# Performance work log

Measured on AMD Instinct MI355X. Metric: run time of the kernel, lower is better.

The kernel has to match this reference:

```python
import jax, jax.numpy as jnp
import numpy as np

C = 512
H = 8
D = C // H
GROUPS = 32
EPS = 1e-5

def setup_inputs() -> dict:
    key = jax.random.key(0)
    ks = jax.random.split(key, 7)
    B, L = 4, 2048
    x = jax.random.normal(ks[0], (B, C, L), dtype=jnp.float32)
    gamma = jnp.ones((C,), dtype=jnp.float32)
    beta = jnp.zeros((C,), dtype=jnp.float32)
    w_qkv = jax.random.normal(ks[1], (3 * C, C), dtype=jnp.float32) * (1.0 / np.sqrt(C))
    b_qkv = jax.random.normal(ks[2], (3 * C,), dtype=jnp.float32) * 0.01
    w_proj = jax.random.normal(ks[3], (C, C), dtype=jnp.float32) * (1.0 / np.sqrt(C))
    b_proj = jax.random.normal(ks[4], (C,), dtype=jnp.float32) * 0.01
    return {"x": x, "gamma": gamma, "beta": beta, "w_qkv": w_qkv,
            "b_qkv": b_qkv, "w_proj": w_proj, "b_proj": b_proj}

def _group_norm(x, gamma, beta):
    B, Cc, L = x.shape
    xg = x.reshape(B, GROUPS, Cc // GROUPS, L)
    mean = jnp.mean(xg, axis=(2, 3), keepdims=True)
    var = jnp.var(xg, axis=(2, 3), keepdims=True)
    xn = ((xg - mean) * jax.lax.rsqrt(var + EPS)).reshape(B, Cc, L)
    return xn * gamma[None, :, None] + beta[None, :, None]

def reference(x, gamma, beta, w_qkv, b_qkv, w_proj, b_proj):
    B, Cc, L = x.shape
    h = _group_norm(x, gamma, beta)
    # 1x1 conv == channel matmul: (3C,C) x (B,C,L) -> (B,3C,L)
    qkv = jnp.einsum('oc,bcl->bol', w_qkv, h) + b_qkv[None, :, None]
    q, k, v = jnp.split(qkv, 3, axis=1)
    # (B,C,L) -> (B,H,L,D)
    def to_heads(t):
        return t.reshape(B, H, D, L).transpose(0, 1, 3, 2)
    q, k, v = to_heads(q), to_heads(k), to_heads(v)
    scale = 1.0 / np.sqrt(D).astype(np.float32)
    attn = jnp.einsum('bhqd,bhkd->bhqk', q, k) * scale  # [B,H,L,L]
    attn = jax.nn.softmax(attn, axis=-1)
    out = jnp.einsum('bhqk,bhkd->bhqd', attn, v)  # [B,H,L,D]
    out = out.transpose(0, 1, 3, 2).reshape(B, Cc, L)
    proj = jnp.einsum('oc,bcl->bol', w_proj, out) + b_proj[None, :, None]
    return x + proj
```

## Files before the change

kernel.cpp:

```cpp
#include <hip/hip_runtime.h>
#include <stdint.h>

#define C_DIM 512
#define H_HEADS 8
#define D_HEAD 64
#define B_BATCH 4
#define L_SEQ 2048
#define GROUPS 32
#define EPS_GN 1e-5f

typedef unsigned short u16;
typedef __attribute__((ext_vector_type(8))) __bf16 bf16x8;
typedef __attribute__((ext_vector_type(2))) float f32x2;
typedef __attribute__((ext_vector_type(4))) float f32x4;
typedef __attribute__((ext_vector_type(16))) float f32x16;

__device__ __forceinline__ u16 f2bf(float f) {
  unsigned u = __builtin_bit_cast(unsigned, f);
  unsigned r = u + 0x7FFFu + ((u >> 16) & 1u);
  return (u16)(r >> 16);
}

__device__ __forceinline__ unsigned cvtpk_bf16(float lo, float hi) {
  unsigned r;
  asm("v_cvt_pk_bf16_f32 %0, %1, %2" : "=v"(r) : "v"(lo), "v"(hi));
  return r;
}

__device__ __forceinline__ void pl32swap(unsigned& a, unsigned& b) {
  asm("v_permlane32_swap_b32 %0, %1" : "+v"(a), "+v"(b));
}

__device__ __forceinline__ bf16x8 mk8(unsigned a, unsigned b, unsigned c, unsigned d) {
  union { uint4 u; bf16x8 v; } z;
  z.u.x = a; z.u.y = b; z.u.z = c; z.u.w = d;
  return z.v;
}

__device__ __forceinline__ void gl16(const void* g, void* l) {
  __builtin_amdgcn_global_load_lds((const __attribute__((address_space(1))) void*)g,
                                   (__attribute__((address_space(3))) void*)l, 16, 0, 0);
}

__global__ __launch_bounds__(256) void prep_kernel(const float* __restrict__ x,
                                                   const float* __restrict__ gamma,
                                                   const float* __restrict__ beta,
                                                   const float* __restrict__ wq,
                                                   const float* __restrict__ wp,
                                                   u16* __restrict__ h_t,
                                                   u16* __restrict__ wq_bf,
                                                   u16* __restrict__ wp_bf) {
  if (blockIdx.x >= 128) {
    int i = (blockIdx.x - 128) * 256 + threadIdx.x;
    const int nq = 3 * C_DIM * C_DIM;
    int idx = i * 4;
    const float* src;
    u16* dst;
    if (idx < nq) { src = wq + idx; dst = wq_bf + idx; }
    else          { src = wp + (idx - nq); dst = wp_bf + (idx - nq); }
    float4 v = *(const float4*)src;
    uint2 pk;
    pk.x = cvtpk_bf16(v.x, v.y);
    pk.y = cvtpk_bf16(v.z, v.w);
    *(uint2*)dst = pk;
    return;
  }
  int bg = blockIdx.x;
  int b = bg >> 5, g = bg & 31;
  const float* base = x + ((size_t)(b * C_DIM + g * 16)) * L_SEQ;
  int t = threadIdx.x;
  int w = t >> 6;
  float s = 0.f, sq = 0.f;
  for (int i = 0; i < 32; ++i) {
    float4 v = ((const float4*)base)[t + i * 256];
    s += v.x + v.y + v.z + v.w;
    sq += v.x * v.x + v.y * v.y + v.z * v.z + v.w * v.w;
  }
  for (int off = 32; off; off >>= 1) { s += __shfl_down(s, off); sq += __shfl_down(sq, off); }
  __shared__ float red[8];
  if ((t & 63) == 0) { red[w * 2] = s; red[w * 2 + 1] = sq; }
  __syncthreads();
  float ts = red[0] + red[2] + red[4] + red[6];
  float tq = red[1] + red[3] + red[5] + red[7];
  float mean = ts * (1.f / 32768.f);
  float var = tq * (1.f / 32768.f) - mean * mean;
  float rstd = rsqrtf(var + EPS_GN);
  float ga[16], be[16];
#pragma unroll
  for (int c = 0; c < 16; ++c) {
    float gm = gamma[g * 16 + c];
    ga[c] = gm * rstd;
    be[c] = beta[g * 16 + c] - mean * gm * rstd;
  }
  __shared__ float tile[16][260];
  for (int lc = 0; lc < 8; ++lc) {
    __syncthreads();
#pragma unroll
    for (int it = 0; it < 4; ++it) {
      int r = it * 4 + w;
      int c4 = (t & 63) * 4;
      *(float4*)&tile[r][c4] = *(const float4*)(base + (size_t)r * L_SEQ + lc * 256 + c4);
    }
    __syncthreads();
    int l = lc * 256 + t;
    unsigned wds[8];
#pragma unroll
    for (int c = 0; c < 8; ++c) {
      float a0 = tile[2 * c][t] * ga[2 * c] + be[2 * c];
      float a1 = tile[2 * c + 1][t] * ga[2 * c + 1] + be[2 * c + 1];
      wds[c] = cvtpk_bf16(a0, a1);
    }
    u16* dst = h_t + ((size_t)(b * L_SEQ + l)) * C_DIM + g * 16;
    uint4 p0; p0.x = wds[0]; p0.y = wds[1]; p0.z = wds[2]; p0.w = wds[3];
    uint4 p1; p1.x = wds[4]; p1.y = wds[5]; p1.z = wds[6]; p1.w = wds[7];
    *(uint4*)dst = p0;
    *(uint4*)(dst + 8) = p1;
  }
}

__global__ __launch_bounds__(256) void gemm_qkv(const u16* __restrict__ A_bf,
                                                const u16* __restrict__ B_t,
                                                const float* __restrict__ bias,
                                                u16* __restrict__ q_t,
                                                u16* __restrict__ kf_g,
                                                u16* __restrict__ vf_g) {
  constexpr int K = 512;
  __shared__ u16 A_lds[128][32];
  __shared__ u16 B_lds[128][32];
  int t = threadIdx.x;
  int w = t >> 6, lane = t & 63;
  int q4 = lane >> 4, c15 = lane & 15;
  int wm = w >> 1, wn = w & 1;
  int o0 = blockIdx.y * 128;
  int l0 = blockIdx.x * 128;
  int b = blockIdx.z;
  const u16* Bb = B_t + (size_t)b * L_SEQ * K;
  f32x4 acc[4][4] = {};

  int sr = lane >> 2, sc = lane & 3;
  int r0 = w * 32 + sr;
  int r1 = r0 + 16;
  int lc0 = (sc - (r0 >> 1)) & 3;
  int lc1 = (sc - (r1 >> 1)) & 3;
  const u16* Ag0 = A_bf + (size_t)(o0 + r0) * K + lc0 * 8;
  const u16* Ag1 = A_bf + (size_t)(o0 + r1) * K + lc1 * 8;
  const u16* Bg0 = Bb + (size_t)(l0 + r0) * K + lc0 * 8;
  const u16* Bg1 = Bb + (size_t)(l0 + r1) * K + lc1 * 8;
  u16* Al0 = &A_lds[w * 32][0];
  u16* Al1 = &A_lds[w * 32 + 16][0];
  u16* Bl0 = &B_lds[w * 32][0];
  u16* Bl1 = &B_lds[w * 32 + 16][0];

  for (int kt = 0; kt < K / 32; ++kt) {
    gl16(Ag0, Al0); gl16(Ag1, Al1);
    gl16(Bg0, Bl0); gl16(Bg1, Bl1);
    Ag0 += 32; Ag1 += 32; Bg0 += 32; Bg1 += 32;
    __syncthreads();
    bf16x8 af[4], bfr[4];
#pragma unroll
    for (int mi = 0; mi < 4; ++mi) {
      int ar = wm * 64 + mi * 16 + c15;
      af[mi] = *(const bf16x8*)&A_lds[ar][((q4 + (ar >> 1)) & 3) * 8];
    }
#pragma unroll
    for (int ni = 0; ni < 4; ++ni) {
      int br = wn * 64 + ni * 16 + c15;
      bfr[ni] = *(const bf16x8*)&B_lds[br][((q4 + (br >> 1)) & 3) * 8];
    }
#pragma unroll
    for (int mi = 0; mi < 4; ++mi)
#pragma unroll
      for (int ni = 0; ni < 4; ++ni)
        acc[mi][ni] = __builtin_amdgcn_mfma_f32_16x16x32_bf16(af[mi], bfr[ni], acc[mi][ni], 0, 0, 0);
    __syncthreads();
  }

  const float QS = 0.18033688f;
  int sel = o0 >> 9;
  int ob = o0 - sel * 512 + wm * 64;
#pragma unroll
  for (int mi = 0; mi < 4; ++mi) {
    int orow = ob + mi * 16 + q4 * 4;
    float4 bi = *(const float4*)&bias[o0 + wm * 64 + mi * 16 + q4 * 4];
#pragma unroll
    for (int ni = 0; ni < 4; ++ni) {
      int l = l0 + wn * 64 + ni * 16 + c15;
      float v0 = acc[mi][ni][0] + bi.x;
      float v1 = acc[mi][ni][1] + bi.y;
      float v2 = acc[mi][ni][2] + bi.z;
      float v3 = acc[mi][ni][3] + bi.w;
      if (sel == 0) {
        v0 *= QS; v1 *= QS; v2 *= QS; v3 *= QS;
        uint2 pk;
        pk.x = cvtpk_bf16(v0, v1);
        pk.y = cvtpk_bf16(v2, v3);
        *(uint2*)(q_t + ((size_t)(b * L_SEQ + l)) * C_DIM + orow) = pk;
      } else if (sel == 1) {
        int hh = orow >> 6, d = orow & 63;
        size_t base = ((size_t)(b * 8 + hh)) * 131072 +
                      (size_t)(((l >> 5) * 4 + (d >> 4))) * 512 +
                      (size_t)((l & 31) + ((d >> 3) & 1) * 32) * 8 + (d & 7);
        uint2 pk;
        pk.x = cvtpk_bf16(v0, v1);
        pk.y = cvtpk_bf16(v2, v3);
        *(uint2*)(kf_g + base) = pk;
      } else {
        int hh = orow >> 6, d = orow & 63;
        size_t base0 = ((size_t)(b * 8 + hh)) * 131072 +
                       (size_t)(l >> 4) * 1024 +
                       (size_t)((l >> 3) & 1) * 256 + (l & 7);
        vf_g[base0 + (size_t)((d + 0) >> 5) * 512 + ((d + 0) & 31) * 8] = f2bf(v0);
        vf_g[base0 + (size_t)((d + 1) >> 5) * 512 + ((d + 1) & 31) * 8] = f2bf(v1);
        vf_g[base0 + (size_t)((d + 2) >> 5) * 512 + ((d + 2) & 31) * 8] = f2bf(v2);
        vf_g[base0 + (size_t)((d + 3) >> 5) * 512 + ((d + 3) & 31) * 8] = f2bf(v3);
      }
    }
  }
}

__global__ __launch_bounds__(256) void gemm_proj(const u16* __restrict__ A_bf,
                                                 const u16* __restrict__ B_t,
                                                 const float* __restrict__ bias,
                                                 const float* __restrict__ xres,
                                                 float* __restrict__ out_f) {
  constexpr int K = 512;
  __shared__ u16 A_lds[64][32];
  __shared__ u16 B_lds[128][32];
  int t = threadIdx.x;
  int w = t >> 6, lane = t & 63;
  int q4 = lane >> 4, c15 = lane & 15;
  int o0 = blockIdx.y * 64;
  int l0 = blockIdx.x * 128;
  int b = blockIdx.z;
  const u16* Bb = B_t + (size_t)b * L_SEQ * K;
  f32x4 acc[4][2] = {};

  int sr = lane >> 2, sc = lane & 3;
  int ra = w * 16 + sr;
  int lca = (sc - (ra >> 1)) & 3;
  const u16* Ag = A_bf + (size_t)(o0 + ra) * K + lca * 8;
  int rb0 = w * 32 + sr, rb1 = rb0 + 16;
  int lcb0 = (sc - (rb0 >> 1)) & 3;
  int lcb1 = (sc - (rb1 >> 1)) & 3;
  const u16* Bg0 = Bb + (size_t)(l0 + rb0) * K + lcb0 * 8;
  const u16* Bg1 = Bb + (size_t)(l0 + rb1) * K + lcb1 * 8;
  u16* Al = &A_lds[w * 16][0];
  u16* Bl0 = &B_lds[w * 32][0];
  u16* Bl1 = &B_lds[w * 32 + 16][0];

  for (int kt = 0; kt < K / 32; ++kt) {
    gl16(Ag, Al);
    gl16(Bg0, Bl0); gl16(Bg1, Bl1);
    Ag += 32; Bg0 += 32; Bg1 += 32;
    __syncthreads();
    bf16x8 af[4], bfr[2];
#pragma unroll
    for (int mi = 0; mi < 4; ++mi) {
      int ar = mi * 16 + c15;
      af[mi] = *(const bf16x8*)&A_lds[ar][((q4 + (ar >> 1)) & 3) * 8];
    }
#pragma unroll
    for (int ni = 0; ni < 2; ++ni) {
      int br = w * 32 + ni * 16 + c15;
      bfr[ni] = *(const bf16x8*)&B_lds[br][((q4 + (br >> 1)) & 3) * 8];
    }
#pragma unroll
    for (int mi = 0; mi < 4; ++mi)
#pragma unroll
      for (int ni = 0; ni < 2; ++ni)
        acc[mi][ni] = __builtin_amdgcn_mfma_f32_16x16x32_bf16(af[mi], bfr[ni], acc[mi][ni], 0, 0, 0);
    __syncthreads();
  }

#pragma unroll
  for (int mi = 0; mi < 4; ++mi) {
    int orow = o0 + mi * 16 + q4 * 4;
    float4 bi = *(const float4*)&bias[orow];
#pragma unroll
    for (int ni = 0; ni < 2; ++ni) {
      int l = l0 + w * 32 + ni * 16 + c15;
      size_t base2 = ((size_t)(b * C_DIM + orow)) * L_SEQ + l;
      out_f[base2] = acc[mi][ni][0] + bi.x + xres[base2];
      out_f[base2 + L_SEQ] = acc[mi][ni][1] + bi.y + xres[base2 + L_SEQ];
      out_f[base2 + 2 * L_SEQ] = acc[mi][ni][2] + bi.z + xres[base2 + 2 * L_SEQ];
      out_f[base2 + 3 * L_SEQ] = acc[mi][ni][3] + bi.w + xres[base2 + 3 * L_SEQ];
    }
  }
}

#define ATILE(KC, KN, T)                                                       \
  {                                                                            \
    int tn = (T) + 1; tn = tn > 31 ? 31 : tn;                                  \
    const u16* kp = kfb + tn * 2048;                                           \
    const u16* vp = vfb + (T) * 2048;                                          \
    KN[0] = *(const bf16x8*)(kp);                                              \
    KN[1] = *(const bf16x8*)(kp + 512);                                        \
    KN[2] = *(const bf16x8*)(kp + 1024);                                       \
    KN[3] = *(const bf16x8*)(kp + 1536);                                       \
    bf16x8 v0 = *(const bf16x8*)(vp);                                          \
    bf16x8 v1 = *(const bf16x8*)(vp + 512);                                    \
    bf16x8 v2 = *(const bf16x8*)(vp + 1024);                                   \
    bf16x8 v3 = *(const bf16x8*)(vp + 1536);                                   \
    f32x16 s;                                                                  \
    _Pragma("unroll") for (int r = 0; r < 16; ++r) s[r] = 0.f;                 \
    s = __builtin_amdgcn_mfma_f32_32x32x16_bf16(KC[0], qf[0], s, 0, 0, 0);     \
    s = __builtin_amdgcn_mfma_f32_32x32x16_bf16(KC[1], qf[1], s, 0, 0, 0);     \
    s = __builtin_amdgcn_mfma_f32_32x32x16_bf16(KC[2], qf[2], s, 0, 0, 0);     \
    s = __builtin_amdgcn_mfma_f32_32x32x16_bf16(KC[3], qf[3], s, 0, 0, 0);     \
    _Pragma("unroll") for (int r = 0; r < 16; ++r)                             \
        s[r] = __builtin_amdgcn_exp2f(s[r]);                                   \
    f32x2 a0_ = {s[0], s[1]}, a1_ = {s[2], s[3]}, a2_ = {s[4], s[5]},          \
          a3_ = {s[6], s[7]}, a4_ = {s[8], s[9]}, a5_ = {s[10], s[11]},        \
          a6_ = {s[12], s[13]}, a7_ = {s[14], s[15]};                          \
    f32x2 b0_ = a0_ + a1_, b1_ = a2_ + a3_, b2_ = a4_ + a5_, b3_ = a6_ + a7_;  \
    f32x2 c0_ = b0_ + b1_, c1_ = b2_ + b3_;                                    \
    f32x2 d0_ = c0_ + c1_;                                                     \
    float sum = d0_[0] + d0_[1];                                               \
    sum += __shfl_xor(sum, 32);                                                \
    l_r += sum;                                                                \
    unsigned pk[8];                                                            \
    _Pragma("unroll") for (int i = 0; i < 8; ++i)                              \
        pk[i] = cvtpk_bf16(s[2 * i], s[2 * i + 1]);                            \
    pl32swap(pk[0], pk[2]); pl32swap(pk[1], pk[3]);                            \
    pl32swap(pk[4], pk[6]); pl32swap(pk[5], pk[7]);                            \
    bf16x8 pf0 = mk8(pk[0], pk[1], pk[2], pk[3]);                              \
    bf16x8 pf1 = mk8(pk[4], pk[5], pk[6], pk[7]);                              \
    o0 = __builtin_amdgcn_mfma_f32_32x32x16_bf16(v0, pf0, o0, 0, 0, 0);        \
    o1 = __builtin_amdgcn_mfma_f32_32x32x16_bf16(v1, pf0, o1, 0, 0, 0);        \
    o0 = __builtin_amdgcn_mfma_f32_32x32x16_bf16(v2, pf1, o0, 0, 0, 0);        \
    o1 = __builtin_amdgcn_mfma_f32_32x32x16_bf16(v3, pf1, o1, 0, 0, 0);        \
  }

__global__ __launch_bounds__(256, 4) void attn_kernel(const u16* __restrict__ q_t,
                                                      const u16* __restrict__ kf_g,
                                                      const u16* __restrict__ vf_g,
                                                      u16* __restrict__ ao_t) {
  __shared__ float oL[4][64][32];
  __shared__ float lL[4][32];

  int g = blockIdx.x;
  int wk = (g & 7) * 128 + (g >> 3);
  int qg = wk & 31, bh = wk >> 5;
  int b = bh >> 3, h = bh & 7;
  int t = threadIdx.x;
  int wv = t >> 6, lane = t & 63;
  int q = lane & 31, hi = lane >> 5;
  int qh = wv & 1, kvh = wv >> 1;
  int q0 = qg * 64 + qh * 32;

  const u16* qp = q_t + ((size_t)(b * L_SEQ + q0 + q)) * C_DIM + h * 64 + hi * 8;
  bf16x8 qf[4];
#pragma unroll
  for (int kk = 0; kk < 4; ++kk) qf[kk] = *(const bf16x8*)(qp + kk * 16);

  const u16* kfb = kf_g + (size_t)bh * 131072 + (size_t)kvh * 65536 + lane * 8;
  const u16* vfb = vf_g + (size_t)bh * 131072 + (size_t)kvh * 65536 + lane * 8;

  f32x16 o0, o1;
#pragma unroll
  for (int r = 0; r < 16; ++r) { o0[r] = 0.f; o1[r] = 0.f; }
  float l_r = 0.f;

  bf16x8 kA[4], kB[4];
#pragma unroll
  for (int i = 0; i < 4; ++i) kA[i] = *(const bf16x8*)(kfb + i * 512);

  for (int it = 0; it < 16; ++it) {
    ATILE(kA, kB, 2 * it);
    ATILE(kB, kA, 2 * it + 1);
  }

  if (hi == 0) lL[wv][q] = l_r;
#pragma unroll
  for (int r = 0; r < 16; ++r) {
    int d = (r & 3) + 8 * (r >> 2) + 4 * hi;
    oL[wv][d][q] = o0[r];
    oL[wv][d + 32][q] = o1[r];
  }
  __syncthreads();

  int tq = t & 31;
  int oqh = (t >> 5) & 1;
  int d0 = (t >> 6) * 16;
  float lsum = lL[oqh][tq] + lL[oqh + 2][tq];
  float inv = 1.f / lsum;
  float v[16];
#pragma unroll
  for (int i = 0; i < 16; ++i)
    v[i] = (oL[oqh][d0 + i][tq] + oL[oqh + 2][d0 + i][tq]) * inv;
  u16* dst = ao_t + ((size_t)(b * L_SEQ + qg * 64 + oqh * 32 + tq)) * C_DIM + h * 64 + d0;
  uint4 ov0, ov1;
  ov0.x = cvtpk_bf16(v[0], v[1]);
  ov0.y = cvtpk_bf16(v[2], v[3]);
  ov0.z = cvtpk_bf16(v[4], v[5]);
  ov0.w = cvtpk_bf16(v[6], v[7]);
  ov1.x = cvtpk_bf16(v[8], v[9]);
  ov1.y = cvtpk_bf16(v[10], v[11]);
  ov1.z = cvtpk_bf16(v[12], v[13]);
  ov1.w = cvtpk_bf16(v[14], v[15]);
  *(uint4*)dst = ov0;
  *(uint4*)(dst + 8) = ov1;
}

extern "C" void kernel_launch(void* const* d_in, const int* in_sizes, int n_in,
                              void* d_out, int out_size, void* d_ws, size_t ws_size,
                              hipStream_t stream) {
  const float* x = (const float*)d_in[0];
  const float* gamma = (const float*)d_in[1];
  const float* beta = (const float*)d_in[2];
  const float* w_qkv = (const float*)d_in[3];
  const float* b_qkv = (const float*)d_in[4];
  const float* w_proj = (const float*)d_in[5];
  const float* b_proj = (const float*)d_in[6];
  float* out = (float*)d_out;

  u16* wq_bf = (u16*)d_ws;
  u16* wp_bf = wq_bf + 786432;
  u16* h_t = wp_bf + 262144;
  u16* q_t = h_t + 4194304;
  u16* kf_g = q_t + 4194304;
  u16* vf_g = kf_g + 4194304;
  u16* ao_t = vf_g + 4194304;

  prep_kernel<<<dim3(1152), dim3(256), 0, stream>>>(x, gamma, beta, w_qkv, w_proj,
                                                    h_t, wq_bf, wp_bf);
  gemm_qkv<<<dim3(16, 12, 4), dim3(256), 0, stream>>>(wq_bf, h_t, b_qkv, q_t, kf_g, vf_g);
  attn_kernel<<<dim3(1024), dim3(256), 0, stream>>>(q_t, kf_g, vf_g, ao_t);
  gemm_proj<<<dim3(16, 8, 4), dim3(256), 0, stream>>>(wp_bf, ao_t, b_proj, x, out);
}
```

Baseline: 103.4 us.

## Software-pipeline QK^T one tile ahead of softmax/PV in attention loop

Restructures the attention inner loop so the QK^T MFMAs for tile T+1 are issued while exp2, row-sum and PV MFMAs for tile T run, and K loads are prefetched two tiles ahead. The goal is to hide MFMA latency and exp/convert dependency chains behind independent matrix work. It keeps an extra 16-float score accumulator live, and launch bounds drop from 4 to 3 waves per SIMD to make room for the registers, which lowers occupancy.

Result: no change. 103.8 us (+0.5%).

```diff
diff --git a/kernel.cpp b/kernel.cpp
--- a/kernel.cpp
+++ b/kernel.cpp
@@ -288,30 +288,30 @@
   }
 }
 
-#define ATILE(KC, KN, T)                                                       \
+#define ABODY(KL, KN, SC, SN, T)                                               \
   {                                                                            \
-    int tn = (T) + 1; tn = tn > 31 ? 31 : tn;                                  \
-    const u16* kp = kfb + tn * 2048;                                           \
+    int tl = (T) + 2; tl = tl > 31 ? 31 : tl;                                  \
+    const u16* kp = kfb + tl * 2048;                                           \
     const u16* vp = vfb + (T) * 2048;                                          \
-    KN[0] = *(const bf16x8*)(kp);                                              \
-    KN[1] = *(const bf16x8*)(kp + 512);                                        \
-    KN[2] = *(const bf16x8*)(kp + 1024);                                       \
-    KN[3] = *(const bf16x8*)(kp + 1536);                                       \
+    KL[0] = *(const bf16x8*)(kp);                                              \
+    KL[1] = *(const bf16x8*)(kp + 512);                                        \
+    KL[2] = *(const bf16x8*)(kp + 1024);                                       \
+    KL[3] = *(const bf16x8*)(kp + 1536);                                       \
+    _Pragma("unroll") for (int r = 0; r < 16; ++r) SN[r] = 0.f;                \
+    SN = __builtin_amdgcn_mfma_f32_32x32x16_bf16(KN[0], qf[0], SN, 0, 0, 0);   \
+    SN = __builtin_amdgcn_mfma_f32_32x32x16_bf16(KN[1], qf[1], SN, 0, 0, 0);   \
+    SN = __builtin_amdgcn_mfma_f32_32x32x16_bf16(KN[2], qf[2], SN, 0, 0, 0);   \
+    SN = __builtin_amdgcn_mfma_f32_32x32x16_bf16(KN[3], qf[3], SN, 0, 0, 0);   \
     bf16x8 v0 = *(const bf16x8*)(vp);                                          \
     bf16x8 v1 = *(const bf16x8*)(vp + 512);                                    \
     bf16x8 v2 = *(const bf16x8*)(vp + 1024);                                   \
     bf16x8 v3 = *(const bf16x8*)(vp + 1536);                                   \
-    f32x16 s;                                                                  \
-    _Pragma("unroll") for (int r = 0; r < 16; ++r) s[r] = 0.f;                 \
-    s = __builtin_amdgcn_mfma_f32_32x32x16_bf16(KC[0], qf[0], s, 0, 0, 0);     \
-    s = __builtin_amdgcn_mfma_f32_32x32x16_bf16(KC[1], qf[1], s, 0, 0, 0);     \
-    s = __builtin_amdgcn_mfma_f32_32x32x16_bf16(KC[2], qf[2], s, 0, 0, 0);     \
-    s = __builtin_amdgcn_mfma_f32_32x32x16_bf16(KC[3], qf[3], s, 0, 0, 0);     \
+    float e[16];                                                               \
     _Pragma("unroll") for (int r = 0; r < 16; ++r)                             \
-        s[r] = __builtin_amdgcn_exp2f(s[r]);                                   \
-    f32x2 a0_ = {s[0], s[1]}, a1_ = {s[2], s[3]}, a2_ = {s[4], s[5]},          \
-          a3_ = {s[6], s[7]}, a4_ = {s[8], s[9]}, a5_ = {s[10], s[11]},        \
-          a6_ = {s[12], s[13]}, a7_ = {s[14], s[15]};                          \
+        e[r] = __builtin_amdgcn_exp2f(SC[r]);                                  \
+    f32x2 a0_ = {e[0], e[1]}, a1_ = {e[2], e[3]}, a2_ = {e[4], e[5]},          \
+          a3_ = {e[6], e[7]}, a4_ = {e[8], e[9]}, a5_ = {e[10], e[11]},        \
+          a6_ = {e[12], e[13]}, a7_ = {e[14], e[15]};                          \
     f32x2 b0_ = a0_ + a1_, b1_ = a2_ + a3_, b2_ = a4_ + a5_, b3_ = a6_ + a7_;  \
     f32x2 c0_ = b0_ + b1_, c1_ = b2_ + b3_;                                    \
     f32x2 d0_ = c0_ + c1_;                                                     \
@@ -320,7 +320,7 @@
     l_r += sum;                                                                \
     unsigned pk[8];                                                            \
     _Pragma("unroll") for (int i = 0; i < 8; ++i)                              \
-        pk[i] = cvtpk_bf16(s[2 * i], s[2 * i + 1]);                            \
+        pk[i] = cvtpk_bf16(e[2 * i], e[2 * i + 1]);                            \
     pl32swap(pk[0], pk[2]); pl32swap(pk[1], pk[3]);                            \
     pl32swap(pk[4], pk[6]); pl32swap(pk[5], pk[7]);                            \
     bf16x8 pf0 = mk8(pk[0], pk[1], pk[2], pk[3]);                              \
@@ -331,7 +331,39 @@
     o1 = __builtin_amdgcn_mfma_f32_32x32x16_bf16(v3, pf1, o1, 0, 0, 0);        \
   }
 
-__global__ __launch_bounds__(256, 4) void attn_kernel(const u16* __restrict__ q_t,
+#define AEPI(SC, T)                                                            \
+  {                                                                            \
+    const u16* vp = vfb + (T) * 2048;                                          \
+    bf16x8 v0 = *(const bf16x8*)(vp);                                          \
+    bf16x8 v1 = *(const bf16x8*)(vp + 512);                                    \
+    bf16x8 v2 = *(const bf16x8*)(vp + 1024);                                   \
+    bf16x8 v3 = *(const bf16x8*)(vp + 1536);                                   \
+    float e[16];                                                               \
+    _Pragma("unroll") for (int r = 0; r < 16; ++r)                             \
+        e[r] = __builtin_amdgcn_exp2f(SC[r]);                                  \
+    f32x2 a0_ = {e[0], e[1]}, a1_ = {e[2], e[3]}, a2_ = {e[4], e[5]},          \
+          a3_ = {e[6], e[7]}, a4_ = {e[8], e[9]}, a5_ = {e[10], e[11]},        \
+          a6_ = {e[12], e[13]}, a7_ = {e[14], e[15]};                          \
+    f32x2 b0_ = a0_ + a1_, b1_ = a2_ + a3_, b2_ = a4_ + a5_, b3_ = a6_ + a7_;  \
+    f32x2 c0_ = b0_ + b1_, c1_ = b2_ + b3_;                                    \
+    f32x2 d0_ = c0_ + c1_;                                                     \
+    float sum = d0_[0] + d0_[1];                                               \
+    sum += __shfl_xor(sum, 32);                                                \
+    l_r += sum;                                                                \
+    unsigned pk[8];                                                            \
+    _Pragma("unroll") for (int i = 0; i < 8; ++i)                              \
+        pk[i] = cvtpk_bf16(e[2 * i], e[2 * i + 1]);                            \
+    pl32swap(pk[0], pk[2]); pl32swap(pk[1], pk[3]);                            \
+    pl32swap(pk[4], pk[6]); pl32swap(pk[5], pk[7]);                            \
+    bf16x8 pf0 = mk8(pk[0], pk[1], pk[2], pk[3]);                              \
+    bf16x8 pf1 = mk8(pk[4], pk[5], pk[6], pk[7]);                              \
+    o0 = __builtin_amdgcn_mfma_f32_32x32x16_bf16(v0, pf0, o0, 0, 0, 0);        \
+    o1 = __builtin_amdgcn_mfma_f32_32x32x16_bf16(v1, pf0, o1, 0, 0, 0);        \
+    o0 = __builtin_amdgcn_mfma_f32_32x32x16_bf16(v2, pf1, o0, 0, 0, 0);        \
+    o1 = __builtin_amdgcn_mfma_f32_32x32x16_bf16(v3, pf1, o1, 0, 0, 0);        \
+  }
+
+__global__ __launch_bounds__(256, 3) void attn_kernel(const u16* __restrict__ q_t,
                                                       const u16* __restrict__ kf_g,
                                                       const u16* __restrict__ vf_g,
                                                       u16* __restrict__ ao_t) {
@@ -363,12 +395,23 @@
 
   bf16x8 kA[4], kB[4];
 #pragma unroll
-  for (int i = 0; i < 4; ++i) kA[i] = *(const bf16x8*)(kfb + i * 512);
-
-  for (int it = 0; it < 16; ++it) {
-    ATILE(kA, kB, 2 * it);
-    ATILE(kB, kA, 2 * it + 1);
-  }
+  for (int i = 0; i < 4; ++i) {
+    kB[i] = *(const bf16x8*)(kfb + i * 512);
+    kA[i] = *(const bf16x8*)(kfb + 2048 + i * 512);
+  }
+  f32x16 sA, sB;
+#pragma unroll
+  for (int r = 0; r < 16; ++r) sA[r] = 0.f;
+#pragma unroll
+  for (int kk = 0; kk < 4; ++kk)
+    sA = __builtin_amdgcn_mfma_f32_32x32x16_bf16(kB[kk], qf[kk], sA, 0, 0, 0);
+
+  for (int it = 0; it < 15; ++it) {
+    ABODY(kB, kA, sA, sB, 2 * it);
+    ABODY(kA, kB, sB, sA, 2 * it + 1);
+  }
+  ABODY(kB, kA, sA, sB, 30);
+  AEPI(sB, 31);
 
   if (hi == 0) lL[wv][q] = l_r;
 #pragma unroll
```
